# Performance work log

Measured on AMD Instinct MI355X. Metric: run time of the kernel, lower is better.

## Reference

```python
import jax, jax.numpy as jnp
import numpy as np

N_NODES = 100000
N_EDGES = 1600000
IN_F, HID_F, OUT_F = 128, 128, 64
BN_EPS = 1e-5


def _glorot(key, shape):
    lim = np.sqrt(6.0 / (shape[0] + shape[1]))
    return jax.random.uniform(key, shape, jnp.float32, -lim, lim)


def setup_inputs() -> dict:
    key = jax.random.key(0)
    ks = jax.random.split(key, 12)
    x = jax.random.normal(ks[0], (N_NODES, IN_F), jnp.float32)
    src = jax.random.randint(ks[1], (N_EDGES,), 0, N_NODES, jnp.int64)
    dst = jax.random.randint(ks[2], (N_EDGES,), 0, N_NODES, jnp.int64)
    dims = [(IN_F, HID_F), (HID_F, HID_F), (HID_F, OUT_F)]
    inp = {"x": x, "src": src, "dst": dst}
    for i, (di, do) in enumerate(dims):
        inp[f"w_self{i}"] = _glorot(ks[3 + 2 * i], (di, do))
        inp[f"w_neigh{i}"] = _glorot(ks[4 + 2 * i], (di, do))
        inp[f"b{i}"] = jnp.zeros((do,), jnp.float32)
    for i in range(2):  # BatchNorm1d(hid) after first two convs
        inp[f"gamma{i}"] = jnp.ones((HID_F,), jnp.float32)
        inp[f"beta{i}"] = jnp.zeros((HID_F,), jnp.float32)
    return inp


def _sage_conv(h, src, dst, w_self, w_neigh, b):
    # mean aggregation over incoming edges: gather src feats, segment-sum by dst
    deg = jax.ops.segment_sum(jnp.ones((src.shape[0],), h.dtype), dst, num_segments=N_NODES)
    agg = jax.ops.segment_sum(h[src], dst, num_segments=N_NODES)
    agg = agg / jnp.maximum(deg, 1.0)[:, None]
    return h @ w_self + agg @ w_neigh + b


def _batchnorm(h, gamma, beta):
    mu = jnp.mean(h, axis=0)
    var = jnp.var(h, axis=0)
    return (h - mu) * jax.lax.rsqrt(var + BN_EPS) * gamma + beta


def reference(x, src, dst, w_self0, w_neigh0, b0, gamma0, beta0,
              w_self1, w_neigh1, b1, gamma1, beta1, w_self2, w_neigh2, b2):
    h = _sage_conv(x, src, dst, w_self0, w_neigh0, b0)
    h = jax.nn.relu(_batchnorm(h, gamma0, beta0))
    h = _sage_conv(h, src, dst, w_self1, w_neigh1, b1)
    h = jax.nn.relu(_batchnorm(h, gamma1, beta1))
    h = _sage_conv(h, src, dst, w_self2, w_neigh2, b2)
    return jax.nn.log_softmax(h, axis=-1)
```

## Files before the change

kernel.cpp:

```cpp
#include <hip/hip_runtime.h>
#include <hip/hip_bf16.h>

typedef unsigned short u16;
typedef unsigned char  u8;
typedef unsigned int   u32;
typedef __attribute__((ext_vector_type(8))) short short8;
typedef __attribute__((ext_vector_type(4))) float floatx4;
typedef __attribute__((ext_vector_type(2))) float floatx2;

__device__ __forceinline__ float bits2f(u32 v){ float f; __builtin_memcpy(&f, &v, 4); return f; }
__device__ __forceinline__ u16 f2bf(float f){
    __hip_bfloat16 h = __float2bfloat16(f);
    u16 u; __builtin_memcpy(&u, &h, 2); return u;
}

__device__ __forceinline__ void gload_lds16(const void* g, void* l){
    __builtin_amdgcn_global_load_lds(
        (const __attribute__((address_space(1))) unsigned char*)g,
        (__attribute__((address_space(3))) unsigned char*)l, 16, 0, 0);
}

#define NBIN 32


__global__ __launch_bounds__(256) void prep_kernel(const float* __restrict__ x,
                                                   u16* __restrict__ hbuf,
                                                   u32* __restrict__ x8, int total4, int nCvtB,
                                                   const int* __restrict__ dst,
                                                   int* __restrict__ gbcnt, int E, int nHistB,
                                                   const float* __restrict__ w0s, const float* __restrict__ w0n,
                                                   const float* __restrict__ w1s, const float* __restrict__ w1n,
                                                   const float* __restrict__ w2s, const float* __restrict__ w2n,
                                                   u16* __restrict__ bp0, u16* __restrict__ bp1,
                                                   u16* __restrict__ bp2){
    const int b = blockIdx.x;
    if (b < nCvtB){
        const int i0 = b * 256 + threadIdx.x;
        const int S  = nCvtB * 256;
        float4 v[4];
        #pragma unroll
        for (int u = 0; u < 4; ++u){
            const int idx = i0 + u * S;
            if (idx < total4) v[u] = ((const float4*)x)[idx];
        }
        #pragma unroll
        for (int u = 0; u < 4; ++u){
            const int idx = i0 + u * S;
            if (idx < total4){
                uint2 o;
                o.x = (u32)f2bf(v[u].x) | ((u32)f2bf(v[u].y) << 16);
                o.y = (u32)f2bf(v[u].z) | ((u32)f2bf(v[u].w) << 16);
                ((uint2*)hbuf)[idx] = o;
                u32 p8 = (u32)__builtin_amdgcn_cvt_pk_fp8_f32(v[u].x, v[u].y, 0, false);
                p8     = (u32)__builtin_amdgcn_cvt_pk_fp8_f32(v[u].z, v[u].w, (int)p8, true);
                x8[idx] = p8;
            }
        }
    } else if (b < nCvtB + nHistB){
        __shared__ int bc[256];
        const int t = threadIdx.x;
        bc[t] = 0;
        __syncthreads();
        const int tile0 = (b - nCvtB) * 8192;
        const int cnt = min(8192, E - tile0);
        for (int j = t; j < cnt; j += 256) atomicAdd(&bc[dst[tile0 + j] >> 9], 1);
        __syncthreads();
        if (bc[t] > 0) atomicAdd(&gbcnt[t], bc[t]);
    } else {
        int i = (b - nCvtB - nHistB) * 256 + threadIdx.x;
        const float *ws, *wn; u16* bp; int N;
        if (i < 32768){ ws = w0s; wn = w0n; bp = bp0; N = 128; }
        else if (i < 65536){ i -= 32768; ws = w1s; wn = w1n; bp = bp1; N = 128; }
        else { i -= 65536; ws = w2s; wn = w2n; bp = bp2; N = 64; }
        int n = i >> 8, k = i & 255;
        float v = (k < 128) ? ws[k * N + n] : wn[(k - 128) * N + n];
        bp[i] = f2bf(v);
    }
}


__global__ __launch_bounds__(256) void cvt8a_kernel(const u16* __restrict__ in,
                                                    const float* __restrict__ cs,
                                                    const float* __restrict__ gamma,
                                                    const float* __restrict__ beta,
                                                    float invM,
                                                    uint2* __restrict__ out8, int total8){
    __shared__ float s_sc[128], s_sh[128];
    if (threadIdx.x < 128){
        const int c = threadIdx.x;
        float s = 0.f, q = 0.f;
        #pragma unroll
        for (int b = 0; b < NBIN; ++b){
            s += cs[b * 256 + c];
            q += cs[b * 256 + 128 + c];
        }
        float mu  = s * invM;
        float var = fmaxf(q * invM - mu * mu, 0.f);
        float sc  = gamma[c] * rsqrtf(var + 1e-5f);
        s_sc[c] = sc;
        s_sh[c] = beta[c] - mu * sc;
    }
    __syncthreads();
    int i = blockIdx.x * 256 + threadIdx.x;
    if (i >= total8) return;
    const int c0 = (i & 15) * 8;
    uint4 v = ((const uint4*)in)[i];
    u32 w[4] = {v.x, v.y, v.z, v.w};
    float f[8];
    #pragma unroll
    for (int j = 0; j < 4; ++j){
        f[2*j]   = bits2f(w[j] << 16);
        f[2*j+1] = bits2f(w[j] & 0xffff0000u);
    }
    #pragma unroll
    for (int j = 0; j < 8; ++j)
        f[j] = fmaxf(fmaf(f[j], s_sc[c0 + j], s_sh[c0 + j]), 0.f);
    u32 lo = (u32)__builtin_amdgcn_cvt_pk_fp8_f32(f[0], f[1], 0, false);
    lo     = (u32)__builtin_amdgcn_cvt_pk_fp8_f32(f[2], f[3], (int)lo, true);
    u32 hi = (u32)__builtin_amdgcn_cvt_pk_fp8_f32(f[4], f[5], 0, false);
    hi     = (u32)__builtin_amdgcn_cvt_pk_fp8_f32(f[6], f[7], (int)hi, true);
    uint2 o; o.x = lo; o.y = hi;
    out8[i] = o;
}


__global__ __launch_bounds__(256) void bscan_kernel(const int* __restrict__ gbcnt,
                                                    int* __restrict__ bbase,
                                                    int* __restrict__ bcur, int nbuk){
    __shared__ int ws[4];
    const int t = threadIdx.x, lane = t & 63, wv = t >> 6;
    int v = (t < nbuk) ? gbcnt[t] : 0;
    int s = v;
    for (int off = 1; off < 64; off <<= 1){
        int n = __shfl_up(s, off);
        if (lane >= off) s += n;
    }
    if (lane == 63) ws[wv] = s;
    __syncthreads();
    int woff = 0;
    for (int w = 0; w < wv; ++w) woff += ws[w];
    int excl = s + woff - v;
    if (t < nbuk){ bbase[t] = excl; bcur[t] = excl; }
}

#define BIN_TILE 8192
__global__ __launch_bounds__(256) void bin_kernel(const int* __restrict__ src,
                                                  const int* __restrict__ dst,
                                                  int* __restrict__ bcur,
                                                  u32* __restrict__ pairs, int E, int nbuk){
    __shared__ u32 hcnt[256], hexcl[256], hoff[256];
    __shared__ int gbase[256];
    __shared__ u32 stage[BIN_TILE];
    __shared__ unsigned char bkt[BIN_TILE];
    const int t = threadIdx.x;
    const int tile0 = blockIdx.x * BIN_TILE;
    const int cntE = min(BIN_TILE, E - tile0);

    hcnt[t] = 0;
    __syncthreads();
    for (int j = t; j < cntE; j += 256){
        int d = dst[tile0 + j];
        atomicAdd(&hcnt[d >> 9], 1u);
    }
    __syncthreads();
    if (t < 64){
        u32 a0 = hcnt[4*t], a1 = hcnt[4*t+1], a2 = hcnt[4*t+2], a3 = hcnt[4*t+3];
        u32 lsum = a0 + a1 + a2 + a3;
        u32 s = lsum;
        for (int off = 1; off < 64; off <<= 1){
            u32 n = __shfl_up(s, off);
            if (t >= off) s += n;
        }
        u32 base = s - lsum;
        hexcl[4*t]   = base;
        hexcl[4*t+1] = base + a0;
        hexcl[4*t+2] = base + a0 + a1;
        hexcl[4*t+3] = base + a0 + a1 + a2;
        hoff[4*t]   = base;
        hoff[4*t+1] = base + a0;
        hoff[4*t+2] = base + a0 + a1;
        hoff[4*t+3] = base + a0 + a1 + a2;
    }
    __syncthreads();
    if (t < nbuk && hcnt[t] > 0) gbase[t] = atomicAdd(&bcur[t], (int)hcnt[t]);
    for (int j = t; j < cntE; j += 256){
        int d = dst[tile0 + j];
        int s = src[tile0 + j];
        int b = d >> 9;
        u32 p = atomicAdd(&hoff[b], 1u);
        stage[p] = ((u32)s << 9) | (u32)(d & 511);
        bkt[p] = (unsigned char)b;
    }
    __syncthreads();
    for (int j = t; j < cntE; j += 256){
        int b = bkt[j];
        pairs[gbase[b] + (int)((u32)j - hexcl[b])] = stage[j];
    }
}

__global__ __launch_bounds__(256) void sort2_kernel(const u32* __restrict__ pairs,
                                                    const int* __restrict__ bbase,
                                                    int* __restrict__ indptr,
                                                    float* __restrict__ invdeg,
                                                    int* __restrict__ esrc,
                                                    int M, int E, int nbuk){
    __shared__ int ndeg[512];
    __shared__ int cur[512];
    __shared__ int wsI[4];
    const int b = blockIdx.x;
    const int node0 = b * 512;
    const int lo = bbase[b];
    const int hi = (b + 1 < nbuk) ? bbase[b + 1] : E;
    const int t = threadIdx.x, lane = t & 63, wv = t >> 6;

    ndeg[t] = 0; ndeg[t + 256] = 0;
    __syncthreads();
    for (int i = lo + t; i < hi; i += 256) atomicAdd(&ndeg[pairs[i] & 511], 1);
    __syncthreads();

    const int d0 = ndeg[2*t], d1 = ndeg[2*t + 1];
    const int p = d0 + d1;
    int s = p;
    for (int off = 1; off < 64; off <<= 1){
        int n = __shfl_up(s, off);
        if (lane >= off) s += n;
    }
    if (lane == 63) wsI[wv] = s;
    __syncthreads();
    int woff = 0;
    for (int w = 0; w < wv; ++w) woff += wsI[w];
    const int incl = s + woff;
    const int excl0 = incl - p;
    const int excl1 = excl0 + d0;

    const int n0 = node0 + 2*t, n1 = node0 + 2*t + 1;
    if (n0 < M){
        indptr[n0 + 1] = lo + excl0 + d0;
        invdeg[n0] = 1.0f / (float)max(d0, 1);
        cur[2*t] = lo + excl0;
    }
    if (n1 < M){
        indptr[n1 + 1] = lo + excl1 + d1;
        invdeg[n1] = 1.0f / (float)max(d1, 1);
        cur[2*t + 1] = lo + excl1;
    }
    if (b == 0 && t == 0) indptr[0] = 0;
    __syncthreads();
    for (int i = lo + t; i < hi; i += 256){
        u32 v = pairs[i];
        int pos = atomicAdd(&cur[v & 511], 1);
        esrc[pos] = (int)(v >> 9);
    }
}


__global__ __launch_bounds__(256) void agg_kernel(const u8* __restrict__ h8,
                                                  const int* __restrict__ indptr,
                                                  const int* __restrict__ esrc,
                                                  const float* __restrict__ invdeg,
                                                  u16* __restrict__ agg, int M){
    const int l8 = threadIdx.x & 7;
    const int n = (blockIdx.x * 256 + threadIdx.x) >> 3;
    if (n >= M) return;
    const int beg = indptr[n];
    const int end = indptr[n + 1];
    const float fs = invdeg[n];

    floatx2 acc[8];
    #pragma unroll
    for (int i = 0; i < 8; ++i){ acc[i].x = 0.f; acc[i].y = 0.f; }

    const u8* hb = h8 + l8 * 16;

    auto accum = [&](uint4 v){
        u32 w[4] = {v.x, v.y, v.z, v.w};
        #pragma unroll
        for (int j = 0; j < 4; ++j){
            acc[2*j]   += __builtin_amdgcn_cvt_pk_f32_fp8(w[j], false);
            acc[2*j+1] += __builtin_amdgcn_cvt_pk_f32_fp8(w[j], true);
        }
    };

    int e = beg;
    for (; e + 8 <= end; e += 8){
        int idx[8];
        #pragma unroll
        for (int u = 0; u < 8; ++u) idx[u] = esrc[e + u];
        uint4 v[8];
        #pragma unroll
        for (int u = 0; u < 8; ++u) v[u] = *(const uint4*)(hb + (size_t)idx[u] * 128);
        #pragma unroll
        for (int u = 0; u < 8; ++u) accum(v[u]);
    }
    if (e + 4 <= end){
        int idx[4];
        #pragma unroll
        for (int u = 0; u < 4; ++u) idx[u] = esrc[e + u];
        uint4 v[4];
        #pragma unroll
        for (int u = 0; u < 4; ++u) v[u] = *(const uint4*)(hb + (size_t)idx[u] * 128);
        #pragma unroll
        for (int u = 0; u < 4; ++u) accum(v[u]);
        e += 4;
    }
    for (; e < end; ++e){
        uint4 v0 = *(const uint4*)(hb + (size_t)esrc[e] * 128);
        accum(v0);
    }

    u32 o[8];
    #pragma unroll
    for (int k = 0; k < 8; ++k)
        o[k] = (u32)f2bf(acc[k].x * fs) | ((u32)f2bf(acc[k].y * fs) << 16);
    uint4 w0 = {o[0], o[1], o[2], o[3]};
    uint4 w1 = {o[4], o[5], o[6], o[7]};
    *(uint4*)(agg + (size_t)n * 128 + l8 * 16)     = w0;
    *(uint4*)(agg + (size_t)n * 128 + l8 * 16 + 8) = w1;
}


template<int NTW, bool STATS, bool AFFA, bool LSM>
__global__ __launch_bounds__(256, 4) void gemm3_kernel(const u16* __restrict__ hA,
                                                       const u16* __restrict__ aggA,
                                                       const u16* __restrict__ Bp,
                                                       const float* __restrict__ bias,
                                                       const float* __restrict__ cs,
                                                       const float* __restrict__ gammaA,
                                                       const float* __restrict__ betaA,
                                                       float invM,
                                                       void* __restrict__ outPre,
                                                       float* __restrict__ csOut,
                                                       int M, int T, int GBs){
    constexpr int N = NTW * 64;
    __shared__ __align__(16) u16 Abuf[3][4096];
    __shared__ __align__(16) char cbuf[4352];
    __shared__ float s_sc[128], s_sh[128];

    const int wave = threadIdx.x >> 6;
    const int lane = threadIdx.x & 63;
    const int m15 = lane & 15;
    const int quad = lane >> 4;
    const int colbase = wave * (NTW * 16);

    if (AFFA && threadIdx.x < 128){
        const int c = threadIdx.x;
        float s = 0.f, q = 0.f;
        #pragma unroll
        for (int b = 0; b < NBIN; ++b){
            s += cs[b * 256 + c];
            q += cs[b * 256 + 128 + c];
        }
        float mu  = s * invM;
        float var = fmaxf(q * invM - mu * mu, 0.f);
        float sc  = gammaA[c] * rsqrtf(var + 1e-5f);
        s_sc[c] = sc;
        s_sh[c] = betaA[c] - mu * sc;
    }
    __syncthreads();

    short8 breg[NTW][8];
    float bv[NTW];
    #pragma unroll
    for (int nt = 0; nt < NTW; ++nt){
        bv[nt] = bias[colbase + nt * 16 + m15];
        #pragma unroll
        for (int k0 = 0; k0 < 8; ++k0)
            breg[nt][k0] = *(const short8*)(Bp + (size_t)(colbase + nt * 16 + m15) * 256 + k0 * 32 + quad * 8);
    }

    float sS[NTW], sQ[NTW];
    #pragma unroll
    for (int nt = 0; nt < NTW; ++nt){ sS[nt] = 0.f; sQ[nt] = 0.f; }

    auto stage = [&](int bufIdx, int tile){
        const int srow = lane & 15, squad = lane >> 4;
        int arow = tile * 16 + srow;
        if (arow >= M) arow = M - 1;
        #pragma unroll
        for (int h = 0; h < 2; ++h){
            const int k0 = wave * 2 + h;
            const u16* base = (k0 < 4) ? hA : aggA;
            const u16* g = base + (size_t)arow * 128 + (k0 & 3) * 32 + squad * 8;
            gload_lds16(g, &Abuf[bufIdx][k0 * 512]);
        }
    };

    const int t0 = blockIdx.x;
    const int nIter = (T - 1 - t0) / GBs + 1;

    stage(0, t0);
    if (nIter > 1) stage(1, t0 + GBs);

    int t = t0;
    for (int it = 0; it < nIter; ++it){
        const int cur = it % 3;
        if (it + 2 < nIter) stage((it + 2) % 3, t + 2 * GBs);

        const int ahead = min(nIter - 1 - it, 2);
        if (ahead >= 2)      asm volatile("s_waitcnt vmcnt(4)" ::: "memory");
        else if (ahead == 1) asm volatile("s_waitcnt vmcnt(2)" ::: "memory");
        else                 asm volatile("s_waitcnt vmcnt(0)" ::: "memory");
        __builtin_amdgcn_s_barrier();
        __builtin_amdgcn_sched_barrier(0);

        floatx4 acc[NTW];
        #pragma unroll
        for (int nt = 0; nt < NTW; ++nt) acc[nt] = 0.0f;
        #pragma unroll
        for (int k0 = 0; k0 < 8; ++k0){
            short8 a = *(const short8*)&Abuf[cur][k0 * 512 + quad * 128 + m15 * 8];
            if (AFFA && k0 < 4){
                const int cb = k0 * 32 + quad * 8;
                #pragma unroll
                for (int j = 0; j < 8; ++j){
                    float f = bits2f(((u32)(u16)a[j]) << 16);
                    f = fmaxf(fmaf(f, s_sc[cb + j], s_sh[cb + j]), 0.f);
                    a[j] = (short)f2bf(f);
                }
            }
            #pragma unroll
            for (int nt = 0; nt < NTW; ++nt)
                acc[nt] = __builtin_amdgcn_mfma_f32_16x16x32_bf16(a, breg[nt][k0], acc[nt], 0, 0, 0);
        }

        const int r0 = quad * 4;
        #pragma unroll
        for (int nt = 0; nt < NTW; ++nt){
            const int col = colbase + nt * 16 + m15;
            #pragma unroll
            for (int r = 0; r < 4; ++r){
                float v = acc[nt][r] + bv[nt];
                if (STATS){
                    int row = t * 16 + r0 + r;
                    if (row < M){
                        sS[nt] += v;
                        sQ[nt] = fmaf(v, v, sQ[nt]);
                    }
                    ((u16*)cbuf)[(r0 + r) * 136 + col] = f2bf(v);
                } else {
                    ((float*)cbuf)[(r0 + r) * 68 + col] = v;
                }
            }
        }
        asm volatile("s_waitcnt lgkmcnt(0)" ::: "memory");
        __builtin_amdgcn_s_barrier();
        __builtin_amdgcn_sched_barrier(0);

        const int srow = threadIdx.x >> 4, seg = threadIdx.x & 15;
        const int grow = t * 16 + srow;
        if (LSM){
            float4 w = *(const float4*)((const float*)cbuf + srow * 68 + seg * 4);
            float m = fmaxf(fmaxf(w.x, w.y), fmaxf(w.z, w.w));
            m = fmaxf(m, __shfl_xor(m, 1));
            m = fmaxf(m, __shfl_xor(m, 2));
            m = fmaxf(m, __shfl_xor(m, 4));
            m = fmaxf(m, __shfl_xor(m, 8));
            float e = __expf(w.x - m) + __expf(w.y - m) + __expf(w.z - m) + __expf(w.w - m);
            e += __shfl_xor(e, 1);
            e += __shfl_xor(e, 2);
            e += __shfl_xor(e, 4);
            e += __shfl_xor(e, 8);
            float lg = m + __logf(e);
            if (grow < M){
                float4 o;
                o.x = w.x - lg; o.y = w.y - lg; o.z = w.z - lg; o.w = w.w - lg;
                *(float4*)((float*)outPre + (size_t)grow * 64 + seg * 4) = o;
            }
        } else if (grow < M){
            if (STATS){
                uint4 w = *(const uint4*)((const u16*)cbuf + srow * 136 + seg * 8);
                *(uint4*)((u16*)outPre + (size_t)grow * N + seg * 8) = w;
            } else {
                float4 w = *(const float4*)((const float*)cbuf + srow * 68 + seg * 4);
                *(float4*)((float*)outPre + (size_t)grow * N + seg * 4) = w;
            }
        }
        t += GBs;
    }

    if (STATS){
        const int binoff = (blockIdx.x & (NBIN - 1)) * 256;
        #pragma unroll
        for (int nt = 0; nt < NTW; ++nt){
            float s = sS[nt], q = sQ[nt];
            s += __shfl_xor(s, 16);  s += __shfl_xor(s, 32);
            q += __shfl_xor(q, 16);  q += __shfl_xor(q, 32);
            if (quad == 0){
                const int c = colbase + nt * 16 + m15;
                atomicAdd(&csOut[binoff + c], s);
                atomicAdd(&csOut[binoff + 128 + c], q);
            }
        }
    }
}


extern "C" void kernel_launch(void* const* d_in, const int* in_sizes, int n_in,
                              void* d_out, int out_size, void* d_ws, size_t ws_size,
                              hipStream_t stream) {
    const float* x   = (const float*)d_in[0];
    const int*   src = (const int*)d_in[1];
    const int*   dst = (const int*)d_in[2];
    const float* wself[3]  = {(const float*)d_in[3], (const float*)d_in[6], (const float*)d_in[9]};
    const float* wneigh[3] = {(const float*)d_in[4], (const float*)d_in[7], (const float*)d_in[10]};
    const float* bias[3]   = {(const float*)d_in[5], (const float*)d_in[8], (const float*)d_in[11]};
    const float* gamma[2]  = {(const float*)d_in[12], (const float*)d_in[14]};
    const float* beta[2]   = {(const float*)d_in[13], (const float*)d_in[15]};

    const int M = in_sizes[0] / 128;
    const int E = in_sizes[1];
    const int NBUK = (M + 511) / 512;
    const int T = (M + 15) / 16;
    const int GB = 1024;
    const float invM = 1.0f / (float)M;

    char* ws = (char*)d_ws;
    size_t off = 0;
    auto alloc = [&](size_t bytes) -> void* {
        void* p = ws + off;
        off = (off + bytes + 511) & ~(size_t)511;
        return p;
    };
    int*   gbcnt    = (int*)alloc(256 * 4);
    float* colstat0 = (float*)alloc(NBIN * 256 * 4);
    float* colstat1 = (float*)alloc(NBIN * 256 * 4);
    const size_t zbytes = off;
    int*   bbase  = (int*)alloc(256 * 4);
    int*   bcur   = (int*)alloc(256 * 4);
    int*   indptr = (int*)alloc((size_t)(M + 1) * 4);
    u32*   pairs  = (u32*)alloc((size_t)E * 4);
    int*   esrc   = (int*)alloc((size_t)E * 4);
    float* invdeg = (float*)alloc((size_t)M * 4);
    u16* bpack0 = (u16*)alloc(128 * 256 * 2);
    u16* bpack1 = (u16*)alloc(128 * 256 * 2);
    u16* bpack2 = (u16*)alloc(64 * 256 * 2);
    u16*   hbuf   = (u16*)alloc((size_t)M * 128 * 2);
    u16*   aggbuf = (u16*)alloc((size_t)M * 128 * 2);
    u16*   preA   = (u16*)alloc((size_t)M * 128 * 2);
    u16*   preB   = (u16*)alloc((size_t)M * 128 * 2);
    u8*    x8     = (u8*)alloc((size_t)M * 128);
    u8*    preA8  = (u8*)alloc((size_t)M * 128);
    u8*    preB8  = (u8*)alloc((size_t)M * 128);

    hipMemsetAsync(ws, 0, zbytes, stream);

    const int total4 = M * 32;
    const int nCvtB  = (total4 + 1023) / 1024;
    const int nHistB = (E + 8191) / 8192;
    prep_kernel<<<nCvtB + nHistB + 320, 256, 0, stream>>>(
        x, hbuf, (u32*)x8, total4, nCvtB,
        dst, gbcnt, E, nHistB,
        wself[0], wneigh[0], wself[1], wneigh[1], wself[2], wneigh[2],
        bpack0, bpack1, bpack2);

    bscan_kernel<<<1, 256, 0, stream>>>(gbcnt, bbase, bcur, NBUK);
    bin_kernel<<<(E + BIN_TILE - 1) / BIN_TILE, 256, 0, stream>>>(src, dst, bcur, pairs, E, NBUK);
    sort2_kernel<<<NBUK, 256, 0, stream>>>(pairs, bbase, indptr, invdeg, esrc, M, E, NBUK);

    agg_kernel<<<(M + 31) / 32, 256, 0, stream>>>(x8, indptr, esrc, invdeg, aggbuf, M);
    gemm3_kernel<2, true, false, false><<<GB, 256, 0, stream>>>(hbuf, aggbuf, bpack0, bias[0],
                                                                nullptr, nullptr, nullptr, invM,
                                                                preA, colstat0, M, T, GB);
    cvt8a_kernel<<<(M * 16 + 255) / 256, 256, 0, stream>>>(preA, colstat0, gamma[0], beta[0], invM,
                                                           (uint2*)preA8, M * 16);

    agg_kernel<<<(M + 31) / 32, 256, 0, stream>>>(preA8, indptr, esrc, invdeg, aggbuf, M);
    gemm3_kernel<2, true, true, false><<<GB, 256, 0, stream>>>(preA, aggbuf, bpack1, bias[1],
                                                               colstat0, gamma[0], beta[0], invM,
                                                               preB, colstat1, M, T, GB);
    cvt8a_kernel<<<(M * 16 + 255) / 256, 256, 0, stream>>>(preB, colstat1, gamma[1], beta[1], invM,
                                                           (uint2*)preB8, M * 16);

    agg_kernel<<<(M + 31) / 32, 256, 0, stream>>>(preB8, indptr, esrc, invdeg, aggbuf, M);
    gemm3_kernel<1, false, true, true><<<GB, 256, 0, stream>>>(preB, aggbuf, bpack2, bias[2],
                                                               colstat1, gamma[1], beta[1], invM,
                                                               d_out, nullptr, M, T, GB);
}
```

Before: 388.1 us.

## Reorder aggregation nodes by degree class to balance wavefront work

Builds a degree histogram during CSR construction, scans it, and scatters node ids into a degree-sorted permutation. The aggregation kernels then process nodes in this order, so lanes in the same wavefront handle similar edge counts and divergence from uneven degrees drops. This adds two small kernels and an indirect lookup. It also loses the sequential locality of indptr, esrc and output accesses across neighbouring threads.

```diff
diff --git a/kernel.cpp b/kernel.cpp
--- a/kernel.cpp
+++ b/kernel.cpp
@@ -203,10 +203,12 @@
                                                     int* __restrict__ indptr,
                                                     float* __restrict__ invdeg,
                                                     int* __restrict__ esrc,
+                                                    int* __restrict__ gdch,
                                                     int M, int E, int nbuk){
     __shared__ int ndeg[512];
     __shared__ int cur[512];
     __shared__ int wsI[4];
+    __shared__ int dh[64];
     const int b = blockIdx.x;
     const int node0 = b * 512;
     const int lo = bbase[b];
@@ -214,6 +216,7 @@
     const int t = threadIdx.x, lane = t & 63, wv = t >> 6;
 
     ndeg[t] = 0; ndeg[t + 256] = 0;
+    if (t < 64) dh[t] = 0;
     __syncthreads();
     for (int i = lo + t; i < hi; i += 256) atomicAdd(&ndeg[pairs[i] & 511], 1);
     __syncthreads();
@@ -238,14 +241,17 @@
         indptr[n0 + 1] = lo + excl0 + d0;
         invdeg[n0] = 1.0f / (float)max(d0, 1);
         cur[2*t] = lo + excl0;
+        atomicAdd(&dh[min(d0, 63)], 1);
     }
     if (n1 < M){
         indptr[n1 + 1] = lo + excl1 + d1;
         invdeg[n1] = 1.0f / (float)max(d1, 1);
         cur[2*t + 1] = lo + excl1;
+        atomicAdd(&dh[min(d1, 63)], 1);
     }
     if (b == 0 && t == 0) indptr[0] = 0;
     __syncthreads();
+    if (t < 64 && dh[t] > 0) atomicAdd(&gdch[t], dh[t]);
     for (int i = lo + t; i < hi; i += 256){
         u32 v = pairs[i];
         int pos = atomicAdd(&cur[v & 511], 1);
@@ -254,14 +260,61 @@
 }
 
 
+__global__ __launch_bounds__(64) void permscan_kernel(const int* __restrict__ gdch,
+                                                      int* __restrict__ dccur){
+    const int t = threadIdx.x;
+    int v = gdch[t];
+    int s = v;
+    for (int off = 1; off < 64; off <<= 1){
+        int n = __shfl_up(s, off);
+        if (t >= off) s += n;
+    }
+    dccur[t] = s - v;
+}
+
+#define PB_TILE 8192
+__global__ __launch_bounds__(256) void permscat_kernel(const int* __restrict__ indptr,
+                                                       int* __restrict__ dccur,
+                                                       int* __restrict__ nodeperm, int M){
+    __shared__ u32 h[64];
+    __shared__ int gb[64];
+    __shared__ u32 hcur[64];
+    const int t = threadIdx.x;
+    const int tile0 = blockIdx.x * PB_TILE;
+    const int cnt = min(PB_TILE, M - tile0);
+    if (t < 64) h[t] = 0;
+    __syncthreads();
+    for (int j = t; j < cnt; j += 256){
+        const int n = tile0 + j;
+        const int deg = indptr[n + 1] - indptr[n];
+        atomicAdd(&h[min(deg, 63)], 1u);
+    }
+    __syncthreads();
+    if (t < 64){
+        gb[t] = (h[t] > 0) ? atomicAdd(&dccur[t], (int)h[t]) : 0;
+        hcur[t] = 0;
+    }
+    __syncthreads();
+    for (int j = t; j < cnt; j += 256){
+        const int n = tile0 + j;
+        const int deg = indptr[n + 1] - indptr[n];
+        const int cls = min(deg, 63);
+        u32 p = atomicAdd(&hcur[cls], 1u);
+        nodeperm[gb[cls] + (int)p] = n;
+    }
+}
+
+
 __global__ __launch_bounds__(256) void agg_kernel(const u8* __restrict__ h8,
                                                   const int* __restrict__ indptr,
                                                   const int* __restrict__ esrc,
                                                   const float* __restrict__ invdeg,
+                                                  const int* __restrict__ nodeperm,
                                                   u16* __restrict__ agg, int M){
     const int l8 = threadIdx.x & 7;
-    const int n = (blockIdx.x * 256 + threadIdx.x) >> 3;
-    if (n >= M) return;
+    const int gid = (blockIdx.x * 256 + threadIdx.x) >> 3;
+    if (gid >= M) return;
+    const int n = nodeperm[gid];
     const int beg = indptr[n];
     const int end = indptr[n + 1];
     const float fs = invdeg[n];
@@ -522,15 +575,18 @@
         return p;
     };
     int*   gbcnt    = (int*)alloc(256 * 4);
+    int*   gdch     = (int*)alloc(64 * 4);
     float* colstat0 = (float*)alloc(NBIN * 256 * 4);
     float* colstat1 = (float*)alloc(NBIN * 256 * 4);
     const size_t zbytes = off;
+    int*   dccur  = (int*)alloc(64 * 4);
     int*   bbase  = (int*)alloc(256 * 4);
     int*   bcur   = (int*)alloc(256 * 4);
     int*   indptr = (int*)alloc((size_t)(M + 1) * 4);
     u32*   pairs  = (u32*)alloc((size_t)E * 4);
     int*   esrc   = (int*)alloc((size_t)E * 4);
     float* invdeg = (float*)alloc((size_t)M * 4);
+    int*   nodeperm = (int*)alloc((size_t)M * 4);
     u16* bpack0 = (u16*)alloc(128 * 256 * 2);
     u16* bpack1 = (u16*)alloc(128 * 256 * 2);
     u16* bpack2 = (u16*)alloc(64 * 256 * 2);
@@ -555,23 +611,25 @@
 
     bscan_kernel<<<1, 256, 0, stream>>>(gbcnt, bbase, bcur, NBUK);
     bin_kernel<<<(E + BIN_TILE - 1) / BIN_TILE, 256, 0, stream>>>(src, dst, bcur, pairs, E, NBUK);
-    sort2_kernel<<<NBUK, 256, 0, stream>>>(pairs, bbase, indptr, invdeg, esrc, M, E, NBUK);
-
-    agg_kernel<<<(M + 31) / 32, 256, 0, stream>>>(x8, indptr, esrc, invdeg, aggbuf, M);
+    sort2_kernel<<<NBUK, 256, 0, stream>>>(pairs, bbase, indptr, invdeg, esrc, gdch, M, E, NBUK);
+    permscan_kernel<<<1, 64, 0, stream>>>(gdch, dccur);
+    permscat_kernel<<<(M + PB_TILE - 1) / PB_TILE, 256, 0, stream>>>(indptr, dccur, nodeperm, M);
+
+    agg_kernel<<<(M + 31) / 32, 256, 0, stream>>>(x8, indptr, esrc, invdeg, nodeperm, aggbuf, M);
     gemm3_kernel<2, true, false, false><<<GB, 256, 0, stream>>>(hbuf, aggbuf, bpack0, bias[0],
                                                                 nullptr, nullptr, nullptr, invM,
                                                                 preA, colstat0, M, T, GB);
     cvt8a_kernel<<<(M * 16 + 255) / 256, 256, 0, stream>>>(preA, colstat0, gamma[0], beta[0], invM,
                                                            (uint2*)preA8, M * 16);
 
-    agg_kernel<<<(M + 31) / 32, 256, 0, stream>>>(preA8, indptr, esrc, invdeg, aggbuf, M);
+    agg_kernel<<<(M + 31) / 32, 256, 0, stream>>>(preA8, indptr, esrc, invdeg, nodeperm, aggbuf, M);
     gemm3_kernel<2, true, true, false><<<GB, 256, 0, stream>>>(preA, aggbuf, bpack1, bias[1],
                                                                colstat0, gamma[0], beta[0], invM,
                                                                preB, colstat1, M, T, GB);
     cvt8a_kernel<<<(M * 16 + 255) / 256, 256, 0, stream>>>(preB, colstat1, gamma[1], beta[1], invM,
                                                            (uint2*)preB8, M * 16);
 
-    agg_kernel<<<(M + 31) / 32, 256, 0, stream>>>(preB8, indptr, esrc, invdeg, aggbuf, M);
+    agg_kernel<<<(M + 31) / 32, 256, 0, stream>>>(preB8, indptr, esrc, invdeg, nodeperm, aggbuf, M);
     gemm3_kernel<1, false, true, true><<<GB, 256, 0, stream>>>(preB, aggbuf, bpack2, bias[2],
                                                                colstat1, gamma[1], beta[1], invM,
                                                                d_out, nullptr, M, T, GB);
```

After: 410.5 us. 5.8% more time.
